# Optimization experiments

Measured on AMD Instinct MI355X. Metric: run time of the kernel, lower is better.

The kernel has to match this reference:

```python
import jax, jax.numpy as jnp
import numpy as np

EMBED_DIM = 768
NUM_HEADS = 12
HEAD_DIM = EMBED_DIM // NUM_HEADS
BSZ = 2
SEQ = 2048


def setup_inputs() -> dict:
    key = jax.random.key(0)
    ks = jax.random.split(key, 8)
    w = lambda k: (jax.random.normal(k, (EMBED_DIM, EMBED_DIM), jnp.float32) * 0.02)
    return {
        "hidden_states": jax.random.normal(ks[0], (BSZ, SEQ, EMBED_DIM), jnp.float32),
        "attention_mask": jnp.zeros((BSZ, 1, SEQ, SEQ), jnp.float32),
        "attention_bias": jax.random.normal(ks[1], (BSZ * NUM_HEADS, SEQ), jnp.float32),
        "Wq": w(ks[2]), "bq": jnp.zeros((EMBED_DIM,), jnp.float32),
        "Wk": w(ks[3]), "bk": jnp.zeros((EMBED_DIM,), jnp.float32),
        "Wv": w(ks[4]), "bv": jnp.zeros((EMBED_DIM,), jnp.float32),
        "Wo": w(ks[5]), "bo": jnp.zeros((EMBED_DIM,), jnp.float32),
        "beta": jnp.ones((1,), jnp.float32),
        "beta_bias": jnp.zeros((1,), jnp.float32),
    }


def reference(hidden_states, attention_mask, attention_bias, Wq, bq, Wk, bk, Wv, bv, Wo, bo, beta, beta_bias):
    b, t, e = hidden_states.shape
    scaling = HEAD_DIM ** -0.5
    split = lambda x: x.reshape(b, t, NUM_HEADS, HEAD_DIM).transpose(0, 2, 1, 3)  # b h t d
    q = split(hidden_states @ Wq.T + bq) * scaling
    k = split(hidden_states @ Wk.T + bk)
    v = split(hidden_states @ Wv.T + bv)
    # scores: [b, h, t, s]
    scores = jnp.einsum('bhqd,bhkd->bhqk', q, k)
    bias = attention_bias.reshape(b, NUM_HEADS, 1, t)  # (bsz*nh, src) -> broadcast over queries
    scores = scores + beta * bias + beta_bias + attention_mask
    probs = jax.nn.softmax(scores, axis=-1)
    out = jnp.einsum('bhqk,bhkd->bhqd', probs, v)  # b h t d
    out = out.transpose(0, 2, 1, 3).reshape(b, t, e)
    return out @ Wo.T + bo
```

## Files before the change

### kernel.cpp

```cpp
#include <hip/hip_runtime.h>
#include <hip/hip_bf16.h>

#define E 768
#define HD 64
#define NH 12
#define BSZ 2
#define SEQ 2048
#define M_ROWS (BSZ * SEQ)
#define BH (BSZ * NH)

#define LOG2E 1.44269504f
#define QSCALE 0.18033688f
#define MSHIFT 16.0f

typedef float f4_t __attribute__((ext_vector_type(4)));
typedef __bf16 bf8_t __attribute__((ext_vector_type(8)));
typedef unsigned short us8_t __attribute__((ext_vector_type(8)));
typedef unsigned short us4_t __attribute__((ext_vector_type(4)));

__device__ inline unsigned short f2bf(float f) {
  union { float f; unsigned u; } v; v.f = f;
  unsigned u = v.u + 0x7FFFu + ((v.u >> 16) & 1u);
  return (unsigned short)(u >> 16);
}

__device__ inline float ex2(float x) { return __builtin_amdgcn_exp2f(x); }

__device__ inline float bflo(unsigned u) { union { unsigned u; float f; } v; v.u = u << 16; return v.f; }
__device__ inline float bfhi(unsigned u) { union { unsigned u; float f; } v; v.u = u & 0xFFFF0000u; return v.f; }

__device__ inline unsigned pk2(float a, float b) {
  union { float f; unsigned u; } ua, ub;
  ua.f = a; ub.f = b;
  return __builtin_amdgcn_perm(ub.u + 0x8000u, ua.u + 0x8000u, 0x07060302u);
}

__global__ __launch_bounds__(256) void cvt_all(
    const float* __restrict__ X, const float* __restrict__ Wq,
    const float* __restrict__ Wk, const float* __restrict__ Wv,
    const float* __restrict__ Wo, const float* __restrict__ mask,
    unsigned short* __restrict__ Xbf, unsigned short* __restrict__ Wqkv,
    unsigned short* __restrict__ Wobf, unsigned short* __restrict__ maskbf) {
  const int nW = E * E;
  int id = blockIdx.x;
  const float* src;
  unsigned short* dst;
  float scale = 1.0f;
  int base;
  if (id < 1536) {
    src = X; dst = Xbf; base = id * 2048;
  } else if (id < 2688) {
    int r = id - 1536;
    int k = r / 288;
    int rb = r - k * 288;
    base = rb * 2048;
    if (k == 0)      { src = Wq; dst = Wqkv;          scale = QSCALE; }
    else if (k == 1) { src = Wk; dst = Wqkv + nW;     }
    else if (k == 2) { src = Wv; dst = Wqkv + 2 * nW; }
    else             { src = Wo; dst = Wobf;          }
  } else {
    src = mask; dst = maskbf; base = (id - 2688) * 2048;
  }
  int i = base + threadIdx.x * 8;
  const float4* s = (const float4*)(src + i);
  float4 a = s[0], b = s[1];
  us8_t o;
  o[0] = f2bf(a.x * scale); o[1] = f2bf(a.y * scale);
  o[2] = f2bf(a.z * scale); o[3] = f2bf(a.w * scale);
  o[4] = f2bf(b.x * scale); o[5] = f2bf(b.y * scale);
  o[6] = f2bf(b.z * scale); o[7] = f2bf(b.w * scale);
  *(us8_t*)(dst + i) = o;
}

__global__ __launch_bounds__(256) void gemm_qkv(
    const unsigned short* __restrict__ A, const unsigned short* __restrict__ Bw,
    const float* __restrict__ bq, const float* __restrict__ bk, const float* __restrict__ bv,
    unsigned short* __restrict__ Qb, unsigned short* __restrict__ Kb,
    unsigned short* __restrict__ Vtb) {
  __shared__ unsigned short Alds[64 * 64];
  __shared__ unsigned short Blds[128 * 64];
  const int w = threadIdx.x >> 6, lane = threadIdx.x & 63;
  const int quad = lane >> 4, l15 = lane & 15;
  const int rowBase = blockIdx.x * 64;
  const int colBase = blockIdx.y * 128;
  const int wr = (w & 1) * 32, wc = (w >> 1) * 64;
  f4_t acc[2][4] = {};
  const int swz = l15 & 7;

  for (int k0 = 0; k0 < E; k0 += 64) {
    __syncthreads();
#pragma unroll
    for (int c = 0; c < 2; ++c) {
      int s = c * 256 + w * 64 + lane;
      int r = s >> 3, col = ((s & 7) ^ (r & 7)) * 8;
      const unsigned short* ga = A + (size_t)(rowBase + r) * E + k0 + col;
      __builtin_amdgcn_global_load_lds((const __attribute__((address_space(1))) void*)ga,
          (__attribute__((address_space(3))) void*)&Alds[c * 2048 + w * 512], 16, 0, 0);
    }
#pragma unroll
    for (int c = 0; c < 4; ++c) {
      int s = c * 256 + w * 64 + lane;
      int r = s >> 3, col = ((s & 7) ^ (r & 7)) * 8;
      const unsigned short* gb = Bw + (size_t)(colBase + r) * E + k0 + col;
      __builtin_amdgcn_global_load_lds((const __attribute__((address_space(1))) void*)gb,
          (__attribute__((address_space(3))) void*)&Blds[c * 2048 + w * 512], 16, 0, 0);
    }
    __builtin_amdgcn_s_waitcnt(0);
    __syncthreads();
    bf8_t af[2][2], bfr[4][2];
#pragma unroll
    for (int mi = 0; mi < 2; ++mi)
#pragma unroll
      for (int ks = 0; ks < 2; ++ks)
        af[mi][ks] = *(const bf8_t*)&Alds[(wr + mi * 16 + l15) * 64 + (((ks * 4 + quad) ^ swz) << 3)];
#pragma unroll
    for (int ni = 0; ni < 4; ++ni)
#pragma unroll
      for (int ks = 0; ks < 2; ++ks)
        bfr[ni][ks] = *(const bf8_t*)&Blds[(wc + ni * 16 + l15) * 64 + (((ks * 4 + quad) ^ swz) << 3)];
#pragma unroll
    for (int ks = 0; ks < 2; ++ks)
#pragma unroll
      for (int mi = 0; mi < 2; ++mi)
#pragma unroll
        for (int ni = 0; ni < 4; ++ni)
          acc[mi][ni] = __builtin_amdgcn_mfma_f32_16x16x32_bf16(af[mi][ks], bfr[ni][ks], acc[mi][ni], 0, 0, 0);
  }

  const int which = colBase / E;
  __syncthreads();
  if (which < 2) {
    const float* biasP = (which == 0) ? bq : bk;
    unsigned short* dst = (which == 0) ? Qb : Kb;
    const float bscale = (which == 0) ? QSCALE : 1.0f;
    const int cnBase = colBase - which * E + wc;
    const int h = cnBase >> 6;
    float biasv[4];
#pragma unroll
    for (int ni = 0; ni < 4; ++ni) biasv[ni] = biasP[cnBase + ni * 16 + l15] * bscale;
    unsigned short* T = Blds + w * 1024;
    const int row = lane >> 2, colE = (lane & 3) * 16;
#pragma unroll
    for (int mi = 0; mi < 2; ++mi) {
#pragma unroll
      for (int ni = 0; ni < 4; ++ni)
#pragma unroll
        for (int r = 0; r < 4; ++r)
          T[(quad * 4 + r) * 64 + ni * 16 + l15] = f2bf(acc[mi][ni][r] + biasv[ni]);
      us8_t o0 = *(const us8_t*)&T[row * 64 + colE];
      us8_t o1 = *(const us8_t*)&T[row * 64 + colE + 8];
      int gm = rowBase + wr + mi * 16 + row;
      int b = gm >> 11, t = gm & 2047;
      unsigned short* drow = dst + ((size_t)(b * NH + h) * SEQ + t) * HD;
      *(us8_t*)&drow[colE] = o0;
      *(us8_t*)&drow[colE + 8] = o1;
    }
  } else {
#pragma unroll
    for (int mi = 0; mi < 2; ++mi) {
#pragma unroll
      for (int ni = 0; ni < 4; ++ni) {
        int cn = colBase - 2 * E + wc + ni * 16 + l15;
        int h = cn >> 6, d = cn & 63;
        float bias = bv[cn];
        int gm0 = rowBase + wr + mi * 16 + quad * 4;
        int b = gm0 >> 11, t = gm0 & 2047;
        us4_t o4;
#pragma unroll
        for (int r = 0; r < 4; ++r) o4[r] = f2bf(acc[mi][ni][r] + bias);
        *(us4_t*)&Vtb[((size_t)(b * NH + h) * HD + d) * SEQ + t] = o4;
      }
    }
  }
}

__global__ __launch_bounds__(256, 4) void flash_attn11(
    const unsigned short* __restrict__ Qb, const unsigned short* __restrict__ Kb,
    const unsigned short* __restrict__ Vt, const float* __restrict__ biasArr,
    const unsigned short* __restrict__ maskB, const float* __restrict__ betaP,
    unsigned short* __restrict__ attn) {
  __shared__ __align__(16) char smem[24576];
  unsigned short* Klds = (unsigned short*)smem;
  unsigned short* Vlds = (unsigned short*)(smem + 8192);
  unsigned short* Plds = (unsigned short*)(smem + 16384);
  const int tid = threadIdx.x;
  const int w = tid >> 6, lane = tid & 63;
  const int quad = lane >> 4, l15 = lane & 15;
  const int id = blockIdx.x;
  const int h = id >> 6;
  const int qb = id & 63;
  const int qt = qb >> 1, b = qb & 1;
  const int bh = b * NH + h;
  const int q0 = qt * 64;
  const int q = q0 + w * 16 + l15;
  const float betav2 = betaP[0] * LOG2E;
  const int sw = l15 & 7;

  const unsigned short* qbase = Qb + ((size_t)bh * SEQ + q) * HD;
  bf8_t qf[2];
  qf[0] = *(const bf8_t*)(qbase + quad * 8);
  qf[1] = *(const bf8_t*)(qbase + 32 + quad * 8);

  union { us8_t u; bf8_t b; } ou;
#pragma unroll
  for (int i = 0; i < 8; ++i) ou.u[i] = 0x3F80;
  const bf8_t ones = ou.b;

  f4_t Oacc[4] = {};
  f4_t Lacc = {};

  unsigned short* Pw = Plds + w * 1024;
  const unsigned short* KgBase = Kb + (size_t)bh * SEQ * HD;
  const unsigned short* VtG = Vt + (size_t)bh * HD * SEQ;
  const unsigned short* maskRow = maskB + ((size_t)b * SEQ + q) * SEQ;
  const float* biasRow = biasArr + (size_t)bh * SEQ;

  const int e0 = tid * 8;
  const int r0 = e0 >> 6, c0 = e0 & 63;
  const int e1 = 2048 + e0;
  const int r1 = e1 >> 6, c1 = e1 & 63;
  const int ph0 = r0 * 64 + ((((c0 >> 3) ^ (r0 & 7))) << 3);
  const int ph1 = r1 * 64 + ((((c1 >> 3) ^ (r1 & 7))) << 3);

  us8_t kreg0, kreg1, vreg0, vreg1;
  uint2 mregu[4];

  {
    const unsigned short* pk0 = KgBase + (size_t)r0 * HD + c0;
    const unsigned short* pk1 = KgBase + (size_t)r1 * HD + c1;
    const unsigned short* pv0 = VtG + (size_t)r0 * SEQ + c0;
    const unsigned short* pv1 = VtG + (size_t)r1 * SEQ + c1;
    asm volatile(
        "global_load_dwordx4 %0, %4, off\n\t"
        "global_load_dwordx4 %1, %5, off\n\t"
        "global_load_dwordx4 %2, %6, off\n\t"
        "global_load_dwordx4 %3, %7, off"
        : "=&v"(kreg0), "=&v"(kreg1), "=&v"(vreg0), "=&v"(vreg1)
        : "v"(pk0), "v"(pk1), "v"(pv0), "v"(pv1));
  }
#pragma unroll
  for (int st = 0; st < 4; ++st)
    mregu[st] = *(const uint2*)&maskRow[st * 16 + quad * 4];

  for (int it = 0; it < 32; ++it) {
    const int soff = it * 64;
    asm volatile("s_waitcnt vmcnt(0)"
                 : "+v"(kreg0), "+v"(kreg1), "+v"(vreg0), "+v"(vreg1));
    __syncthreads();
    *(us8_t*)&Klds[ph0] = kreg0;
    *(us8_t*)&Klds[ph1] = kreg1;
    *(us8_t*)&Vlds[ph0] = vreg0;
    *(us8_t*)&Vlds[ph1] = vreg1;
    __syncthreads();

    float4 bb[4];
#pragma unroll
    for (int st = 0; st < 4; ++st) {
      float4 b4 = *(const float4*)&biasRow[soff + st * 16 + quad * 4];
      bb[st].x = fmaf(betav2, b4.x, -MSHIFT);
      bb[st].y = fmaf(betav2, b4.y, -MSHIFT);
      bb[st].z = fmaf(betav2, b4.z, -MSHIFT);
      bb[st].w = fmaf(betav2, b4.w, -MSHIFT);
    }

    f4_t sacc[4];
#pragma unroll
    for (int st = 0; st < 4; ++st) {
      sacc[st] = (f4_t){0.f, 0.f, 0.f, 0.f};
#pragma unroll
      for (int ks = 0; ks < 2; ++ks) {
        bf8_t kf = *(const bf8_t*)&Klds[(st * 16 + l15) * 64 + (((ks * 4 + quad) ^ sw) << 3)];
        sacc[st] = __builtin_amdgcn_mfma_f32_16x16x32_bf16(kf, qf[ks], sacc[st], 0, 0, 0);
      }
    }

#pragma unroll
    for (int st = 0; st < 4; ++st) {
      sacc[st][0] += fmaf(LOG2E, bflo(mregu[st].x), bb[st].x);
      sacc[st][1] += fmaf(LOG2E, bfhi(mregu[st].x), bb[st].y);
      sacc[st][2] += fmaf(LOG2E, bflo(mregu[st].y), bb[st].z);
      sacc[st][3] += fmaf(LOG2E, bfhi(mregu[st].y), bb[st].w);
    }

    if (it < 31) {
      const int nf = soff + 64;
      const unsigned short* pk0 = KgBase + (size_t)(nf + r0) * HD + c0;
      const unsigned short* pk1 = KgBase + (size_t)(nf + r1) * HD + c1;
      const unsigned short* pv0 = VtG + (size_t)r0 * SEQ + nf + c0;
      const unsigned short* pv1 = VtG + (size_t)r1 * SEQ + nf + c1;
      asm volatile(
          "global_load_dwordx4 %0, %4, off\n\t"
          "global_load_dwordx4 %1, %5, off\n\t"
          "global_load_dwordx4 %2, %6, off\n\t"
          "global_load_dwordx4 %3, %7, off"
          : "=&v"(kreg0), "=&v"(kreg1), "=&v"(vreg0), "=&v"(vreg1)
          : "v"(pk0), "v"(pk1), "v"(pv0), "v"(pv1));
#pragma unroll
      for (int st = 0; st < 4; ++st)
        mregu[st] = *(const uint2*)&maskRow[nf + st * 16 + quad * 4];
    }

#pragma unroll
    for (int st = 0; st < 4; ++st)
#pragma unroll
      for (int r = 0; r < 4; ++r) sacc[st][r] = ex2(sacc[st][r]);

#pragma unroll
    for (int st = 0; st < 4; ++st) {
      uint2 pp;
      pp.x = pk2(sacc[st][0], sacc[st][1]);
      pp.y = pk2(sacc[st][2], sacc[st][3]);
      int col = st * 16 + quad * 4;
      int addr = l15 * 64 + ((((col >> 3) ^ sw)) << 3) + (col & 7);
      *(uint2*)&Pw[addr] = pp;
    }

#pragma unroll
    for (int ks = 0; ks < 2; ++ks) {
      bf8_t pf = *(const bf8_t*)&Pw[l15 * 64 + (((ks * 4 + quad) ^ sw) << 3)];
      Lacc = __builtin_amdgcn_mfma_f32_16x16x32_bf16(ones, pf, Lacc, 0, 0, 0);
#pragma unroll
      for (int dt = 0; dt < 4; ++dt) {
        bf8_t vf = *(const bf8_t*)&Vlds[(dt * 16 + l15) * 64 + (((ks * 4 + quad) ^ sw) << 3)];
        Oacc[dt] = __builtin_amdgcn_mfma_f32_16x16x32_bf16(vf, pf, Oacc[dt], 0, 0, 0);
      }
    }
  }

  float inv = 1.0f / Lacc[0];
  unsigned short* orow = attn + ((size_t)b * SEQ + q) * E + h * HD;
#pragma unroll
  for (int dt = 0; dt < 4; ++dt) {
    us4_t o4;
#pragma unroll
    for (int r = 0; r < 4; ++r) o4[r] = f2bf(Oacc[dt][r] * inv);
    *(us4_t*)&orow[dt * 16 + quad * 4] = o4;
  }
}

__global__ __launch_bounds__(256) void gemm_out(
    const unsigned short* __restrict__ A, const unsigned short* __restrict__ Bw,
    const float* __restrict__ bo, float* __restrict__ out) {
  __shared__ unsigned short Alds[64 * 64];
  __shared__ unsigned short Blds[64 * 64];
  const int w = threadIdx.x >> 6, lane = threadIdx.x & 63;
  const int quad = lane >> 4, l15 = lane & 15;
  const int rowBase = blockIdx.x * 64;
  const int colBase = blockIdx.y * 64;
  const int wr = (w & 1) * 32, wc = (w >> 1) * 32;
  f4_t acc[2][2] = {};
  const int swz = l15 & 7;

  for (int k0 = 0; k0 < E; k0 += 64) {
    __syncthreads();
#pragma unroll
    for (int c = 0; c < 2; ++c) {
      int s = c * 256 + w * 64 + lane;
      int r = s >> 3, col = ((s & 7) ^ (r & 7)) * 8;
      const unsigned short* ga = A + (size_t)(rowBase + r) * E + k0 + col;
      __builtin_amdgcn_global_load_lds((const __attribute__((address_space(1))) void*)ga,
          (__attribute__((address_space(3))) void*)&Alds[c * 2048 + w * 512], 16, 0, 0);
      const unsigned short* gb = Bw + (size_t)(colBase + r) * E + k0 + col;
      __builtin_amdgcn_global_load_lds((const __attribute__((address_space(1))) void*)gb,
          (__attribute__((address_space(3))) void*)&Blds[c * 2048 + w * 512], 16, 0, 0);
    }
    __builtin_amdgcn_s_waitcnt(0);
    __syncthreads();
    bf8_t af[2][2], bfr[2][2];
#pragma unroll
    for (int mi = 0; mi < 2; ++mi)
#pragma unroll
      for (int ks = 0; ks < 2; ++ks)
        af[mi][ks] = *(const bf8_t*)&Alds[(wr + mi * 16 + l15) * 64 + (((ks * 4 + quad) ^ swz) << 3)];
#pragma unroll
    for (int ni = 0; ni < 2; ++ni)
#pragma unroll
      for (int ks = 0; ks < 2; ++ks)
        bfr[ni][ks] = *(const bf8_t*)&Blds[(wc + ni * 16 + l15) * 64 + (((ks * 4 + quad) ^ swz) << 3)];
#pragma unroll
    for (int ks = 0; ks < 2; ++ks)
#pragma unroll
      for (int mi = 0; mi < 2; ++mi)
#pragma unroll
        for (int ni = 0; ni < 2; ++ni)
          acc[mi][ni] = __builtin_amdgcn_mfma_f32_16x16x32_bf16(af[mi][ks], bfr[ni][ks], acc[mi][ni], 0, 0, 0);
  }

#pragma unroll
  for (int mi = 0; mi < 2; ++mi) {
#pragma unroll
    for (int ni = 0; ni < 2; ++ni) {
      int gn = colBase + wc + ni * 16 + l15;
      float bias = bo[gn];
#pragma unroll
      for (int r = 0; r < 4; ++r) {
        int gm = rowBase + wr + mi * 16 + quad * 4 + r;
        out[(size_t)gm * E + gn] = acc[mi][ni][r] + bias;
      }
    }
  }
}

extern "C" void kernel_launch(void* const* d_in, const int* in_sizes, int n_in,
                              void* d_out, int out_size, void* d_ws, size_t ws_size,
                              hipStream_t stream) {
  const float* hidden = (const float*)d_in[0];
  const float* mask = (const float*)d_in[1];
  const float* abias = (const float*)d_in[2];
  const float* Wq = (const float*)d_in[3];
  const float* bq = (const float*)d_in[4];
  const float* Wk = (const float*)d_in[5];
  const float* bk = (const float*)d_in[6];
  const float* Wv = (const float*)d_in[7];
  const float* bv = (const float*)d_in[8];
  const float* Wo = (const float*)d_in[9];
  const float* bo = (const float*)d_in[10];
  const float* beta = (const float*)d_in[11];
  float* out = (float*)d_out;

  char* ws = (char*)d_ws;
  unsigned short* Xbf = (unsigned short*)(ws);
  unsigned short* Wqkv = (unsigned short*)(ws + 6291456);
  unsigned short* Wobf = (unsigned short*)(ws + 9830400);
  unsigned short* Qbuf = (unsigned short*)(ws + 11010048);
  unsigned short* Kbuf = (unsigned short*)(ws + 17301504);
  unsigned short* Vtb = (unsigned short*)(ws + 23592960);
  unsigned short* Maskbf = (unsigned short*)(ws + 29884416);
  unsigned short* Attn = Xbf;

  cvt_all<<<6784, 256, 0, stream>>>(hidden, Wq, Wk, Wv, Wo, mask, Xbf, Wqkv, Wobf, Maskbf);
  gemm_qkv<<<dim3(64, 18), 256, 0, stream>>>(Xbf, Wqkv, bq, bk, bv, Qbuf, Kbuf, Vtb);
  flash_attn11<<<768, 256, 0, stream>>>(Qbuf, Kbuf, Vtb, abias, Maskbf, beta, Attn);
  gemm_out<<<dim3(64, 12), 256, 0, stream>>>(Attn, Wobf, bo, out);
}
```

Before: 227.5 us.

## Rewrite flash attention with 32x32 MFMA, split-KV waves, prepacked mask and bias

The attention kernel now uses 32x32x16 bf16 MFMAs with P kept in registers via permlane32 swaps instead of an LDS round trip. It also splits the key range across two wave pairs that are reduced through LDS at the end, and double-buffers K/V/mask prefetch with partial waitcnts. The conversion kernel pre-scales the mask by log2e and repacks it into an MFMA-friendly tiled layout, and precomputes beta*bias+beta_bias, which fixes the previously ignored beta_bias. The aim is fewer LDS passes, less per-element arithmetic and better MFMA utilisation, at the cost of more registers (occupancy bound lowered to 3) and extra LDS for the final reduction.

New measurement: 194.6 us. 14.5% less time.

```diff
diff --git a/kernel.cpp b/kernel.cpp
--- a/kernel.cpp
+++ b/kernel.cpp
@@ -14,6 +14,7 @@
 #define MSHIFT 16.0f
 
 typedef float f4_t __attribute__((ext_vector_type(4)));
+typedef float f32x16 __attribute__((ext_vector_type(16)));
 typedef __bf16 bf8_t __attribute__((ext_vector_type(8)));
 typedef unsigned short us8_t __attribute__((ext_vector_type(8)));
 typedef unsigned short us4_t __attribute__((ext_vector_type(4)));
@@ -35,41 +36,80 @@
   return __builtin_amdgcn_perm(ub.u + 0x8000u, ua.u + 0x8000u, 0x07060302u);
 }
 
+__device__ inline void swap32(unsigned& a, unsigned& b) {
+  asm volatile("v_permlane32_swap_b32 %0, %1" : "+v"(a), "+v"(b));
+}
+
 __global__ __launch_bounds__(256) void cvt_all(
     const float* __restrict__ X, const float* __restrict__ Wq,
     const float* __restrict__ Wk, const float* __restrict__ Wv,
     const float* __restrict__ Wo, const float* __restrict__ mask,
+    const float* __restrict__ abias, const float* __restrict__ betaP,
+    const float* __restrict__ bbiasP,
     unsigned short* __restrict__ Xbf, unsigned short* __restrict__ Wqkv,
-    unsigned short* __restrict__ Wobf, unsigned short* __restrict__ maskbf) {
+    unsigned short* __restrict__ Wobf, unsigned short* __restrict__ maskbf,
+    float* __restrict__ biasPf) {
   const int nW = E * E;
   int id = blockIdx.x;
-  const float* src;
-  unsigned short* dst;
-  float scale = 1.0f;
-  int base;
-  if (id < 1536) {
-    src = X; dst = Xbf; base = id * 2048;
-  } else if (id < 2688) {
-    int r = id - 1536;
-    int k = r / 288;
-    int rb = r - k * 288;
-    base = rb * 2048;
-    if (k == 0)      { src = Wq; dst = Wqkv;          scale = QSCALE; }
-    else if (k == 1) { src = Wk; dst = Wqkv + nW;     }
-    else if (k == 2) { src = Wv; dst = Wqkv + 2 * nW; }
-    else             { src = Wo; dst = Wobf;          }
-  } else {
-    src = mask; dst = maskbf; base = (id - 2688) * 2048;
-  }
-  int i = base + threadIdx.x * 8;
-  const float4* s = (const float4*)(src + i);
-  float4 a = s[0], b = s[1];
-  us8_t o;
-  o[0] = f2bf(a.x * scale); o[1] = f2bf(a.y * scale);
-  o[2] = f2bf(a.z * scale); o[3] = f2bf(a.w * scale);
-  o[4] = f2bf(b.x * scale); o[5] = f2bf(b.y * scale);
-  o[6] = f2bf(b.z * scale); o[7] = f2bf(b.w * scale);
-  *(us8_t*)(dst + i) = o;
+  if (id < 2688) {
+    const float* src;
+    unsigned short* dst;
+    float scale = 1.0f;
+    int base;
+    if (id < 1536) {
+      src = X; dst = Xbf; base = id * 2048;
+    } else {
+      int r = id - 1536;
+      int k = r / 288;
+      int rb = r - k * 288;
+      base = rb * 2048;
+      if (k == 0)      { src = Wq; dst = Wqkv;          scale = QSCALE; }
+      else if (k == 1) { src = Wk; dst = Wqkv + nW;     }
+      else if (k == 2) { src = Wv; dst = Wqkv + 2 * nW; }
+      else             { src = Wo; dst = Wobf;          }
+    }
+    int i = base + threadIdx.x * 8;
+    const float4* s = (const float4*)(src + i);
+    float4 a = s[0], b = s[1];
+    us8_t o;
+    o[0] = f2bf(a.x * scale); o[1] = f2bf(a.y * scale);
+    o[2] = f2bf(a.z * scale); o[3] = f2bf(a.w * scale);
+    o[4] = f2bf(b.x * scale); o[5] = f2bf(b.y * scale);
+    o[6] = f2bf(b.z * scale); o[7] = f2bf(b.w * scale);
+    *(us8_t*)(dst + i) = o;
+    return;
+  }
+  if (id < 6784) {
+    int rowid = id - 2688;
+    int bb = rowid >> 11, q = rowid & 2047;
+    int s0 = threadIdx.x * 8;
+    const float4* s = (const float4*)(mask + (size_t)rowid * 2048 + s0);
+    float4 a = s[0], c = s[1];
+    int tile = s0 >> 6, kk = s0 & 63;
+    int base = ((bb * 32 + tile) * 2048 + q) * 64 + (kk >> 5) * 32 + ((kk & 31) >> 3) * 4;
+    us4_t lo, hi4;
+    lo[0] = f2bf(a.x * LOG2E); lo[1] = f2bf(a.y * LOG2E);
+    lo[2] = f2bf(a.z * LOG2E); lo[3] = f2bf(a.w * LOG2E);
+    hi4[0] = f2bf(c.x * LOG2E); hi4[1] = f2bf(c.y * LOG2E);
+    hi4[2] = f2bf(c.z * LOG2E); hi4[3] = f2bf(c.w * LOG2E);
+    *(us4_t*)(maskbf + base) = lo;
+    *(us4_t*)(maskbf + base + 16) = hi4;
+    return;
+  }
+  {
+    int bh = id - 6784;
+    int s0 = threadIdx.x * 8;
+    const float4* s = (const float4*)(abias + (size_t)bh * 2048 + s0);
+    float4 a = s[0], c = s[1];
+    float bv = LOG2E * betaP[0];
+    float bc = LOG2E * bbiasP[0] - MSHIFT;
+    int tile = s0 >> 6, kk = s0 & 63;
+    int base = bh * 2048 + tile * 64 + (kk >> 5) * 32 + ((kk & 31) >> 3) * 4;
+    f4_t lo = {fmaf(bv, a.x, bc), fmaf(bv, a.y, bc), fmaf(bv, a.z, bc), fmaf(bv, a.w, bc)};
+    f4_t hi4 = {fmaf(bv, c.x, bc), fmaf(bv, c.y, bc), fmaf(bv, c.z, bc), fmaf(bv, c.w, bc)};
+    *(f4_t*)(biasPf + base) = lo;
+    *(f4_t*)(biasPf + base + 16) = hi4;
+  }
 }
 
 __global__ __launch_bounds__(256) void gemm_qkv(
@@ -174,167 +214,209 @@
   }
 }
 
-__global__ __launch_bounds__(256, 4) void flash_attn11(
+__device__ inline void addBM(f32x16& SA, const float* bp, us8_t ma, us8_t mb) {
+  union { us8_t s; unsigned u[4]; } ca, cb;
+  ca.s = ma; cb.s = mb;
+#pragma unroll
+  for (int g = 0; g < 4; ++g) {
+    f4_t bw = *(const f4_t*)(bp + g * 4);
+    unsigned wl = (g < 2) ? ca.u[2 * g] : cb.u[2 * g - 4];
+    unsigned wh = (g < 2) ? ca.u[2 * g + 1] : cb.u[2 * g - 3];
+    SA[4 * g + 0] += bw[0] + bflo(wl);
+    SA[4 * g + 1] += bw[1] + bfhi(wl);
+    SA[4 * g + 2] += bw[2] + bflo(wh);
+    SA[4 * g + 3] += bw[3] + bfhi(wh);
+  }
+}
+
+__device__ inline void packP(f32x16& SA, float& L, bf8_t& F0, bf8_t& F1) {
+#pragma unroll
+  for (int r = 0; r < 16; ++r) {
+    SA[r] = ex2(SA[r]);
+    L += SA[r];
+  }
+  unsigned u0 = pk2(SA[0], SA[1]), u1 = pk2(SA[2], SA[3]);
+  unsigned u2 = pk2(SA[4], SA[5]), u3 = pk2(SA[6], SA[7]);
+  unsigned u4 = pk2(SA[8], SA[9]), u5 = pk2(SA[10], SA[11]);
+  unsigned u6 = pk2(SA[12], SA[13]), u7 = pk2(SA[14], SA[15]);
+  swap32(u0, u2); swap32(u1, u3); swap32(u4, u6); swap32(u5, u7);
+  union { unsigned u[4]; bf8_t b; } fa, fb;
+  fa.u[0] = u0; fa.u[1] = u1; fa.u[2] = u2; fa.u[3] = u3;
+  fb.u[0] = u4; fb.u[1] = u5; fb.u[2] = u6; fb.u[3] = u7;
+  F0 = fa.b; F1 = fb.b;
+}
+
+__global__ __launch_bounds__(256, 3) void flash_attn12(
     const unsigned short* __restrict__ Qb, const unsigned short* __restrict__ Kb,
-    const unsigned short* __restrict__ Vt, const float* __restrict__ biasArr,
-    const unsigned short* __restrict__ maskB, const float* __restrict__ betaP,
-    unsigned short* __restrict__ attn) {
-  __shared__ __align__(16) char smem[24576];
-  unsigned short* Klds = (unsigned short*)smem;
-  unsigned short* Vlds = (unsigned short*)(smem + 8192);
-  unsigned short* Plds = (unsigned short*)(smem + 16384);
+    const unsigned short* __restrict__ Vt, const unsigned short* __restrict__ maskP,
+    const float* __restrict__ biasPf, unsigned short* __restrict__ attn) {
+  __shared__ __align__(16) char smem[40960];
   const int tid = threadIdx.x;
   const int w = tid >> 6, lane = tid & 63;
-  const int quad = lane >> 4, l15 = lane & 15;
+  const int l31 = lane & 31, hi = lane >> 5;
+  const int p = w >> 1, qw = (w & 1) * 32;
   const int id = blockIdx.x;
   const int h = id >> 6;
   const int qb = id & 63;
   const int qt = qb >> 1, b = qb & 1;
   const int bh = b * NH + h;
   const int q0 = qt * 64;
-  const int q = q0 + w * 16 + l15;
-  const float betav2 = betaP[0] * LOG2E;
-  const int sw = l15 & 7;
-
-  const unsigned short* qbase = Qb + ((size_t)bh * SEQ + q) * HD;
-  bf8_t qf[2];
-  qf[0] = *(const bf8_t*)(qbase + quad * 8);
-  qf[1] = *(const bf8_t*)(qbase + 32 + quad * 8);
-
-  union { us8_t u; bf8_t b; } ou;
-#pragma unroll
-  for (int i = 0; i < 8; ++i) ou.u[i] = 0x3F80;
-  const bf8_t ones = ou.b;
-
-  f4_t Oacc[4] = {};
-  f4_t Lacc = {};
-
-  unsigned short* Pw = Plds + w * 1024;
+  const int q = q0 + qw + l31;
+
+  unsigned short* KldsP = (unsigned short*)(smem + p * 16384);
+  unsigned short* VldsP = KldsP + 4096;
+  float* biasF = (float*)(smem + 32768);
+
+  {
+    const float* srcB = biasPf + bh * 2048 + tid * 8;
+    f4_t b0 = *(const f4_t*)srcB;
+    f4_t b1 = *(const f4_t*)(srcB + 4);
+    *(f4_t*)&biasF[tid * 8] = b0;
+    *(f4_t*)&biasF[tid * 8 + 4] = b1;
+  }
+
+  bf8_t qf[4];
+  {
+    const unsigned short* qbase = Qb + ((size_t)bh * SEQ + q) * HD + hi * 8;
+#pragma unroll
+    for (int dk = 0; dk < 4; ++dk) qf[dk] = *(const bf8_t*)(qbase + dk * 16);
+  }
+
+  const int li = (w & 1) * 64 + lane;
+  const int r0 = li >> 3, cc = li & 7;
+  const int dstOff = r0 * 64 + ((cc ^ (r0 & 7)) << 3);
   const unsigned short* KgBase = Kb + (size_t)bh * SEQ * HD;
   const unsigned short* VtG = Vt + (size_t)bh * HD * SEQ;
-  const unsigned short* maskRow = maskB + ((size_t)b * SEQ + q) * SEQ;
-  const float* biasRow = biasArr + (size_t)bh * SEQ;
-
-  const int e0 = tid * 8;
-  const int r0 = e0 >> 6, c0 = e0 & 63;
-  const int e1 = 2048 + e0;
-  const int r1 = e1 >> 6, c1 = e1 & 63;
-  const int ph0 = r0 * 64 + ((((c0 >> 3) ^ (r0 & 7))) << 3);
-  const int ph1 = r1 * 64 + ((((c1 >> 3) ^ (r1 & 7))) << 3);
-
-  us8_t kreg0, kreg1, vreg0, vreg1;
-  uint2 mregu[4];
-
+  const unsigned short* kSrc = KgBase + (p * 1024 + r0) * 64 + cc * 8;
+  const unsigned short* vSrc = VtG + r0 * SEQ + p * 1024 + cc * 8;
+  const unsigned short* mSrc = maskP + (((size_t)(b * 32 + p * 16) * 2048) + q) * 64 + hi * 16;
+
+  us8_t kpf0, kpf1, kpf2, kpf3, vpf0, vpf1, vpf2, vpf3, mpf0, mpf1, mpf2, mpf3;
+
+#define PF_KV(T)                                                              \
+  {                                                                           \
+    const unsigned short* kp_ = kSrc + (T) * 4096;                            \
+    const unsigned short* vp_ = vSrc + (T) * 64;                              \
+    asm volatile("global_load_dwordx4 %0, %4, off\n\t"                        \
+                 "global_load_dwordx4 %1, %5, off\n\t"                        \
+                 "global_load_dwordx4 %2, %6, off\n\t"                        \
+                 "global_load_dwordx4 %3, %7, off"                            \
+                 : "=&v"(kpf0), "=&v"(kpf1), "=&v"(kpf2), "=&v"(kpf3)         \
+                 : "v"(kp_), "v"(kp_ + 1024), "v"(kp_ + 2048), "v"(kp_ + 3072)); \
+    asm volatile("global_load_dwordx4 %0, %4, off\n\t"                        \
+                 "global_load_dwordx4 %1, %5, off\n\t"                        \
+                 "global_load_dwordx4 %2, %6, off\n\t"                        \
+                 "global_load_dwordx4 %3, %7, off"                            \
+                 : "=&v"(vpf0), "=&v"(vpf1), "=&v"(vpf2), "=&v"(vpf3)         \
+                 : "v"(vp_), "v"(vp_ + 16 * SEQ), "v"(vp_ + 32 * SEQ),        \
+                   "v"(vp_ + 48 * SEQ));                                      \
+  }
+
+#define PF_M(T)                                                               \
+  {                                                                           \
+    const unsigned short* mp_ = mSrc + (size_t)(T) * 131072;                  \
+    asm volatile("global_load_dwordx4 %0, %4, off\n\t"                        \
+                 "global_load_dwordx4 %1, %5, off\n\t"                        \
+                 "global_load_dwordx4 %2, %6, off\n\t"                        \
+                 "global_load_dwordx4 %3, %7, off"                            \
+                 : "=&v"(mpf0), "=&v"(mpf1), "=&v"(mpf2), "=&v"(mpf3)         \
+                 : "v"(mp_), "v"(mp_ + 8), "v"(mp_ + 32), "v"(mp_ + 40));     \
+  }
+
+  PF_KV(0);
+  PF_M(0);
+
+  f32x16 Oacc0 = {}, Oacc1 = {};
+  float Lacc = 0.0f;
+  const int swzA = l31 & 7;
+
+  for (int it = 0; it < 16; ++it) {
+    asm volatile("s_waitcnt vmcnt(4)"
+                 : "+v"(kpf0), "+v"(kpf1), "+v"(kpf2), "+v"(kpf3),
+                   "+v"(vpf0), "+v"(vpf1), "+v"(vpf2), "+v"(vpf3));
+    __syncthreads();
+    {
+      us8_t* kd = (us8_t*)(KldsP + dstOff);
+      kd[0] = kpf0; kd[128] = kpf1; kd[256] = kpf2; kd[384] = kpf3;
+      us8_t* vd = (us8_t*)(VldsP + dstOff);
+      vd[0] = vpf0; vd[128] = vpf1; vd[256] = vpf2; vd[384] = vpf3;
+    }
+    __syncthreads();
+
+    f32x16 s0 = {}, s1 = {};
+    __builtin_amdgcn_s_setprio(1);
+#pragma unroll
+    for (int dk = 0; dk < 4; ++dk) {
+      const int co = ((dk * 2 + hi) ^ swzA) << 3;
+      bf8_t k0 = *(const bf8_t*)(KldsP + l31 * 64 + co);
+      bf8_t k1 = *(const bf8_t*)(KldsP + (32 + l31) * 64 + co);
+      s0 = __builtin_amdgcn_mfma_f32_32x32x16_bf16(k0, qf[dk], s0, 0, 0, 0);
+      s1 = __builtin_amdgcn_mfma_f32_32x32x16_bf16(k1, qf[dk], s1, 0, 0, 0);
+    }
+    __builtin_amdgcn_s_setprio(0);
+
+    if (it < 15) {
+      PF_KV(it + 1);
+      asm volatile("s_waitcnt vmcnt(8)"
+                   : "+v"(mpf0), "+v"(mpf1), "+v"(mpf2), "+v"(mpf3));
+    } else {
+      asm volatile("s_waitcnt vmcnt(0)"
+                   : "+v"(mpf0), "+v"(mpf1), "+v"(mpf2), "+v"(mpf3));
+    }
+
+    const float* bp = biasF + ((p << 4) + it) * 64 + (hi << 4);
+    addBM(s0, bp, mpf0, mpf1);
+    addBM(s1, bp + 32, mpf2, mpf3);
+
+    if (it < 15) PF_M(it + 1);
+
+    bf8_t pfr0, pfr1, pfr2, pfr3;
+    packP(s0, Lacc, pfr0, pfr1);
+    packP(s1, Lacc, pfr2, pfr3);
+
+    __builtin_amdgcn_s_setprio(1);
+#pragma unroll
+    for (int ks = 0; ks < 4; ++ks) {
+      const int co = ((ks * 2 + hi) ^ swzA) << 3;
+      bf8_t v0 = *(const bf8_t*)(VldsP + l31 * 64 + co);
+      bf8_t v1 = *(const bf8_t*)(VldsP + (32 + l31) * 64 + co);
+      bf8_t pp = ks == 0 ? pfr0 : ks == 1 ? pfr1 : ks == 2 ? pfr2 : pfr3;
+      Oacc0 = __builtin_amdgcn_mfma_f32_32x32x16_bf16(v0, pp, Oacc0, 0, 0, 0);
+      Oacc1 = __builtin_amdgcn_mfma_f32_32x32x16_bf16(v1, pp, Oacc1, 0, 0, 0);
+    }
+    __builtin_amdgcn_s_setprio(0);
+  }
+
+  __syncthreads();
   {
-    const unsigned short* pk0 = KgBase + (size_t)r0 * HD + c0;
-    const unsigned short* pk1 = KgBase + (size_t)r1 * HD + c1;
-    const unsigned short* pv0 = VtG + (size_t)r0 * SEQ + c0;
-    const unsigned short* pv1 = VtG + (size_t)r1 * SEQ + c1;
-    asm volatile(
-        "global_load_dwordx4 %0, %4, off\n\t"
-        "global_load_dwordx4 %1, %5, off\n\t"
-        "global_load_dwordx4 %2, %6, off\n\t"
-        "global_load_dwordx4 %3, %7, off"
-        : "=&v"(kreg0), "=&v"(kreg1), "=&v"(vreg0), "=&v"(vreg1)
-        : "v"(pk0), "v"(pk1), "v"(pv0), "v"(pv1));
-  }
-#pragma unroll
-  for (int st = 0; st < 4; ++st)
-    mregu[st] = *(const uint2*)&maskRow[st * 16 + quad * 4];
-
-  for (int it = 0; it < 32; ++it) {
-    const int soff = it * 64;
-    asm volatile("s_waitcnt vmcnt(0)"
-                 : "+v"(kreg0), "+v"(kreg1), "+v"(vreg0), "+v"(vreg1));
-    __syncthreads();
-    *(us8_t*)&Klds[ph0] = kreg0;
-    *(us8_t*)&Klds[ph1] = kreg1;
-    *(us8_t*)&Vlds[ph0] = vreg0;
-    *(us8_t*)&Vlds[ph1] = vreg1;
-    __syncthreads();
-
-    float4 bb[4];
-#pragma unroll
-    for (int st = 0; st < 4; ++st) {
-      float4 b4 = *(const float4*)&biasRow[soff + st * 16 + quad * 4];
-      bb[st].x = fmaf(betav2, b4.x, -MSHIFT);
-      bb[st].y = fmaf(betav2, b4.y, -MSHIFT);
-      bb[st].z = fmaf(betav2, b4.z, -MSHIFT);
-      bb[st].w = fmaf(betav2, b4.w, -MSHIFT);
-    }
-
-    f4_t sacc[4];
-#pragma unroll
-    for (int st = 0; st < 4; ++st) {
-      sacc[st] = (f4_t){0.f, 0.f, 0.f, 0.f};
-#pragma unroll
-      for (int ks = 0; ks < 2; ++ks) {
-        bf8_t kf = *(const bf8_t*)&Klds[(st * 16 + l15) * 64 + (((ks * 4 + quad) ^ sw) << 3)];
-        sacc[st] = __builtin_amdgcn_mfma_f32_16x16x32_bf16(kf, qf[ks], sacc[st], 0, 0, 0);
-      }
-    }
-
-#pragma unroll
-    for (int st = 0; st < 4; ++st) {
-      sacc[st][0] += fmaf(LOG2E, bflo(mregu[st].x), bb[st].x);
-      sacc[st][1] += fmaf(LOG2E, bfhi(mregu[st].x), bb[st].y);
-      sacc[st][2] += fmaf(LOG2E, bflo(mregu[st].y), bb[st].z);
-      sacc[st][3] += fmaf(LOG2E, bfhi(mregu[st].y), bb[st].w);
-    }
-
-    if (it < 31) {
-      const int nf = soff + 64;
-      const unsigned short* pk0 = KgBase + (size_t)(nf + r0) * HD + c0;
-      const unsigned short* pk1 = KgBase + (size_t)(nf + r1) * HD + c1;
-      const unsigned short* pv0 = VtG + (size_t)r0 * SEQ + nf + c0;
-      const unsigned short* pv1 = VtG + (size_t)r1 * SEQ + nf + c1;
-      asm volatile(
-          "global_load_dwordx4 %0, %4, off\n\t"
-          "global_load_dwordx4 %1, %5, off\n\t"
-          "global_load_dwordx4 %2, %6, off\n\t"
-          "global_load_dwordx4 %3, %7, off"
-          : "=&v"(kreg0), "=&v"(kreg1), "=&v"(vreg0), "=&v"(vreg1)
-          : "v"(pk0), "v"(pk1), "v"(pv0), "v"(pv1));
-#pragma unroll
-      for (int st = 0; st < 4; ++st)
-        mregu[st] = *(const uint2*)&maskRow[nf + st * 16 + quad * 4];
-    }
-
-#pragma unroll
-    for (int st = 0; st < 4; ++st)
-#pragma unroll
-      for (int r = 0; r < 4; ++r) sacc[st][r] = ex2(sacc[st][r]);
-
-#pragma unroll
-    for (int st = 0; st < 4; ++st) {
-      uint2 pp;
-      pp.x = pk2(sacc[st][0], sacc[st][1]);
-      pp.y = pk2(sacc[st][2], sacc[st][3]);
-      int col = st * 16 + quad * 4;
-      int addr = l15 * 64 + ((((col >> 3) ^ sw)) << 3) + (col & 7);
-      *(uint2*)&Pw[addr] = pp;
-    }
-
-#pragma unroll
-    for (int ks = 0; ks < 2; ++ks) {
-      bf8_t pf = *(const bf8_t*)&Pw[l15 * 64 + (((ks * 4 + quad) ^ sw) << 3)];
-      Lacc = __builtin_amdgcn_mfma_f32_16x16x32_bf16(ones, pf, Lacc, 0, 0, 0);
-#pragma unroll
-      for (int dt = 0; dt < 4; ++dt) {
-        bf8_t vf = *(const bf8_t*)&Vlds[(dt * 16 + l15) * 64 + (((ks * 4 + quad) ^ sw) << 3)];
-        Oacc[dt] = __builtin_amdgcn_mfma_f32_16x16x32_bf16(vf, pf, Oacc[dt], 0, 0, 0);
-      }
-    }
-  }
-
-  float inv = 1.0f / Lacc[0];
-  unsigned short* orow = attn + ((size_t)b * SEQ + q) * E + h * HD;
-#pragma unroll
-  for (int dt = 0; dt < 4; ++dt) {
-    us4_t o4;
-#pragma unroll
-    for (int r = 0; r < 4; ++r) o4[r] = f2bf(Oacc[dt][r] * inv);
-    *(us4_t*)&orow[dt * 16 + quad * 4] = o4;
+    float* OfP = (float*)smem + p * (64 * 65);
+    const int qr = (qw + l31) * 65;
+#pragma unroll
+    for (int r = 0; r < 16; ++r) {
+      int d = (r & 3) + 8 * (r >> 2) + 4 * hi;
+      OfP[qr + d] = Oacc0[r];
+      OfP[qr + 32 + d] = Oacc1[r];
+    }
+    float Lf = Lacc + __shfl_xor(Lacc, 32);
+    if (hi == 0) OfP[qr + 64] = Lf;
+  }
+  __syncthreads();
+  {
+    const float* O0 = (const float*)smem;
+    const float* O1 = O0 + 64 * 65;
+    const int ql = tid >> 2, dc = tid & 3;
+    const int qr = ql * 65;
+    float inv = 1.0f / (O0[qr + 64] + O1[qr + 64]);
+    unsigned short* orow = attn + ((size_t)b * SEQ + q0 + ql) * E + h * HD + dc * 16;
+    us8_t o0, o1;
+#pragma unroll
+    for (int i = 0; i < 8; ++i)
+      o0[i] = f2bf((O0[qr + dc * 16 + i] + O1[qr + dc * 16 + i]) * inv);
+#pragma unroll
+    for (int i = 0; i < 8; ++i)
+      o1[i] = f2bf((O0[qr + dc * 16 + 8 + i] + O1[qr + dc * 16 + 8 + i]) * inv);
+    *(us8_t*)orow = o0;
+    *(us8_t*)(orow + 8) = o1;
   }
 }
 
@@ -416,6 +498,7 @@
   const float* Wo = (const float*)d_in[9];
   const float* bo = (const float*)d_in[10];
   const float* beta = (const float*)d_in[11];
+  const float* betaBias = (const float*)d_in[12];
   float* out = (float*)d_out;
 
   char* ws = (char*)d_ws;
@@ -426,10 +509,12 @@
   unsigned short* Kbuf = (unsigned short*)(ws + 17301504);
   unsigned short* Vtb = (unsigned short*)(ws + 23592960);
   unsigned short* Maskbf = (unsigned short*)(ws + 29884416);
+  float* BiasP = (float*)(ws + 46661632);
   unsigned short* Attn = Xbf;
 
-  cvt_all<<<6784, 256, 0, stream>>>(hidden, Wq, Wk, Wv, Wo, mask, Xbf, Wqkv, Wobf, Maskbf);
+  cvt_all<<<6808, 256, 0, stream>>>(hidden, Wq, Wk, Wv, Wo, mask, abias, beta, betaBias,
+                                    Xbf, Wqkv, Wobf, Maskbf, BiasP);
   gemm_qkv<<<dim3(64, 18), 256, 0, stream>>>(Xbf, Wqkv, bq, bk, bv, Qbuf, Kbuf, Vtb);
-  flash_attn11<<<768, 256, 0, stream>>>(Qbuf, Kbuf, Vtb, abias, Maskbf, beta, Attn);
+  flash_attn12<<<768, 256, 0, stream>>>(Qbuf, Kbuf, Vtb, Maskbf, BiasP, Attn);
   gemm_out<<<dim3(64, 12), 256, 0, stream>>>(Attn, Wobf, bo, out);
 }
```
